# Optimization experiments

Hardware: AMD Instinct MI355X
Metric: run time of the kernel (lower is better)

Reference implementation:

```python
import jax, jax.numpy as jnp
import numpy as np

B, C, W, H, D = 4, 32, 64, 64, 64


def setup_inputs() -> dict:
    key = jax.random.key(0)
    ks = jax.random.split(key, 8)
    x = jax.random.normal(ks[0], (B, C, W, H, D), dtype=jnp.float32)
    # 1x1x1 Conv3d == per-voxel channel mixing: weight (C_out, C_in), bias (C_out,)
    Wq = jax.random.normal(ks[1], (C, C), dtype=jnp.float32) * 0.05
    bq = jax.random.normal(ks[2], (C,), dtype=jnp.float32) * 0.05
    Wk = jax.random.normal(ks[3], (C, C), dtype=jnp.float32) * 0.05
    bk = jax.random.normal(ks[4], (C,), dtype=jnp.float32) * 0.05
    Wv = jax.random.normal(ks[5], (C, C), dtype=jnp.float32) * 0.05
    bv = jax.random.normal(ks[6], (C,), dtype=jnp.float32) * 0.05
    gamma = jnp.float32(0.1)  # torch inits to 0; nonzero so output depends on attention
    return {"x": x, "Wq": Wq, "bq": bq, "Wk": Wk, "bk": bk, "Wv": Wv, "bv": bv, "gamma": gamma}


def reference(x, Wq, bq, Wk, bk, Wv, bv, gamma):
    b, c, w, h, d = x.shape
    N = w * h * d

    def proj(Wt, bt):
        # 1x1x1 conv then torch's .view(b, -1, c): a raw row-major reshape of
        # (b, c, w, h, d) -> (b, N, c) that interleaves channel/spatial (faithful).
        y = jnp.einsum('oc,bcwhd->bowhd', Wt, x) + bt[None, :, None, None, None]
        return y.reshape(b, N, c)

    q = proj(Wq, bq)  # (b, N, c)
    k = proj(Wk, bk)
    v = proj(Wv, bv)
    s = jnp.einsum('bnc,bnd->bcd', q, k)          # q^T k: tiny (b, c, c)
    a = jax.nn.softmax(s, axis=-1)
    scores = jnp.einsum('bnc,bcd->bnd', v, a)     # (b, N, c)
    return x + gamma * scores.reshape(b, c, w, h, d)
```

## Files before the change

kernel.cpp:

```cpp
#include <hip/hip_runtime.h>

typedef __attribute__((ext_vector_type(8))) short bf16x8;
typedef __attribute__((ext_vector_type(4))) float f32x4;

#define MSP   262144
#define BATCH 4
#define NT    8
#define NBLK  128

#define CSF   264
#define WTILE (8 * CSF)

#define OFF_P  0
#define OFF_CS 4096

#define GLDS16(gsrc, ldst)                                               \
  __builtin_amdgcn_global_load_lds(                                      \
      (const __attribute__((address_space(1))) unsigned int*)(gsrc),     \
      (__attribute__((address_space(3))) unsigned int*)(ldst), 16, 0, 0)

__device__ __forceinline__ unsigned short f2bf(float f) {
  unsigned int u = __float_as_uint(f);
  u += 0x7fffu + ((u >> 16) & 1u);
  return (unsigned short)(u >> 16);
}
__device__ __forceinline__ void split2(float f, short* hi, short* lo) {
  unsigned int u = __float_as_uint(f);
  unsigned int uh = u + (0x7fffu + ((u >> 16) & 1u));
  *hi = (short)(uh >> 16);
  const float r = f - __uint_as_float(uh & 0xffff0000u);
  *lo = (short)(__float_as_uint(r) >> 16);
}

#define MFMA(A, B, C) __builtin_amdgcn_mfma_f32_16x16x32_bf16(A, B, C, 0, 0, 0)


__global__ __launch_bounds__(256) void pass1_kernel(
    const float* __restrict__ x, const float* __restrict__ Wq,
    const float* __restrict__ Wk, float* __restrict__ ws) {
  __shared__ float XT[8 * WTILE];
  __shared__ float UW[3072];
  const int tid = threadIdx.x;
  const int w = tid >> 6, l = tid & 63, lm = tid & 15, lb = (tid >> 4) & 3;
  const int b = blockIdx.y;
  const size_t xbase = (size_t)b * 32 * MSP;
  const int wbase = (blockIdx.x * 4 + w) * (NT * 64);

  const int srow = l >> 4;
  const int scol = (l & 15) * 4;
  float* wbuf0 = XT + (w * 2 + 0) * WTILE;
  float* wbuf1 = XT + (w * 2 + 1) * WTILE;

#pragma unroll
  for (int c = 0; c < 8; ++c)
    GLDS16(x + xbase + (size_t)(c * 4 + srow) * MSP + wbase + scol,
           wbuf0 + c * CSF);

  {
    float* WqL = UW;
    float* WkL = UW + 1024;
    for (int k = tid; k < 1024; k += 256) { WqL[k] = Wq[k]; WkL[k] = Wk[k]; }
    __syncthreads();
    float* UL = UW + 2048;
    for (int k = tid; k < 1024; k += 256) {
      const int aa = k >> 5, bb = k & 31;
      float s = 0.f;
#pragma unroll
      for (int ch = 0; ch < 32; ++ch)
        s = fmaf(WqL[ch * 32 + aa], WkL[ch * 32 + bb], s);
      UL[k] = s;
    }
    __syncthreads();
  }
  bf16x8 uh0, ul0, uh1, ul1;
  {
    const float* UL = UW + 2048;
#pragma unroll
    for (int r = 0; r < 8; ++r) {
      const int kk = (r < 4) ? lb * 4 + r : 16 + lb * 4 + (r - 4);
      short h, lo;
      split2(UL[lm * 32 + kk], &h, &lo);        uh0[r] = h; ul0[r] = lo;
      split2(UL[(16 + lm) * 32 + kk], &h, &lo); uh1[r] = h; ul1[r] = lo;
    }
  }

  int ldsoff[8];
#pragma unroll
  for (int r = 0; r < 8; ++r) {
    const int ch = (r < 4) ? lb * 4 + r : 16 + lb * 4 + (r - 4);
    ldsoff[r] = (ch >> 2) * CSF + (ch & 3) * 64 + lm;
  }

  f32x4 p00 = {0, 0, 0, 0}, p01 = {0, 0, 0, 0}, p10 = {0, 0, 0, 0}, p11 = {0, 0, 0, 0};
  float cs0[8], cs1[8];
#pragma unroll
  for (int r = 0; r < 8; ++r) { cs0[r] = 0.f; cs1[r] = 0.f; }

#pragma unroll 1
  for (int t = 0; t < NT; ++t) {
    const float* XB = (t & 1) ? wbuf1 : wbuf0;
    float* XN = (t & 1) ? wbuf0 : wbuf1;
    if (t + 1 < NT) {
      const int posn = wbase + (t + 1) * 64;
#pragma unroll
      for (int c = 0; c < 8; ++c)
        GLDS16(x + xbase + (size_t)(c * 4 + srow) * MSP + posn + scol,
               XN + c * CSF);
      asm volatile("s_waitcnt vmcnt(8)" ::: "memory");
    } else {
      asm volatile("s_waitcnt vmcnt(0)" ::: "memory");
    }
    __builtin_amdgcn_sched_barrier(0);

#pragma unroll
    for (int g2 = 0; g2 < 2; ++g2) {
      const int pl = g2 * 32;
      float xf0[8], xf1[8];
#pragma unroll
      for (int r = 0; r < 8; ++r) {
        xf0[r] = XB[ldsoff[r] + pl];
        xf1[r] = XB[ldsoff[r] + pl + 16];
      }
      bf16x8 xh0, xl0, xh1, xl1;
#pragma unroll
      for (int r = 0; r < 8; ++r) {
        short h, lo;
        split2(xf0[r], &h, &lo); xh0[r] = h; xl0[r] = lo;
        split2(xf1[r], &h, &lo); xh1[r] = h; xl1[r] = lo;
        cs0[r] += xf0[r];  cs1[r] += xf1[r];
      }

      f32x4 y00 = {0,0,0,0}, y01 = {0,0,0,0}, y10 = {0,0,0,0}, y11 = {0,0,0,0};
      y00 = MFMA(uh0, xh0, y00); y00 = MFMA(uh0, xl0, y00); y00 = MFMA(ul0, xh0, y00);
      y01 = MFMA(uh1, xh0, y01); y01 = MFMA(uh1, xl0, y01); y01 = MFMA(ul1, xh0, y01);
      y10 = MFMA(uh0, xh1, y10); y10 = MFMA(uh0, xl1, y10); y10 = MFMA(ul0, xh1, y10);
      y11 = MFMA(uh1, xh1, y11); y11 = MFMA(uh1, xl1, y11); y11 = MFMA(ul1, xh1, y11);

      bf16x8 yh0, yl0, yh1, yl1;
#pragma unroll
      for (int r = 0; r < 4; ++r) {
        short h, lo;
        split2(y00[r], &h, &lo); yh0[r] = h; yl0[r] = lo;
        split2(y10[r], &h, &lo); yh1[r] = h; yl1[r] = lo;
      }
#pragma unroll
      for (int r = 4; r < 8; ++r) {
        short h, lo;
        split2(y01[r - 4], &h, &lo); yh0[r] = h; yl0[r] = lo;
        split2(y11[r - 4], &h, &lo); yh1[r] = h; yl1[r] = lo;
      }

      p00 = MFMA(xh0, yh0, p00); p00 = MFMA(xh0, yl0, p00); p00 = MFMA(xl0, yh0, p00);
      p01 = MFMA(xh0, yh1, p01); p01 = MFMA(xh0, yl1, p01); p01 = MFMA(xl0, yh1, p01);
      p10 = MFMA(xh1, yh0, p10); p10 = MFMA(xh1, yl0, p10); p10 = MFMA(xl1, yh0, p10);
      p11 = MFMA(xh1, yh1, p11); p11 = MFMA(xh1, yl1, p11); p11 = MFMA(xl1, yh1, p11);
    }
  }

  __syncthreads();
  float* red = XT;
#pragma unroll
  for (int r = 0; r < 4; ++r) {
    red[w * 1024 + (lb * 4 + r) * 32 + lm]           = p00[r];
    red[w * 1024 + (lb * 4 + r) * 32 + 16 + lm]      = p01[r];
    red[w * 1024 + (16 + lb * 4 + r) * 32 + lm]      = p10[r];
    red[w * 1024 + (16 + lb * 4 + r) * 32 + 16 + lm] = p11[r];
  }
  __syncthreads();
  for (int k = tid; k < 1024; k += 256) {
    const float s = red[k] + red[1024 + k] + red[2048 + k] + red[3072 + k];
    atomicAdd(&ws[OFF_P + b * 1024 + k], s);
  }
  __syncthreads();
#pragma unroll
  for (int r = 0; r < 8; ++r) {
    const int ch = (r < 4) ? lb * 4 + r : 16 + lb * 4 + (r - 4);
    red[w * 1024 + ch * 32 + lm]      = cs0[r];
    red[w * 1024 + ch * 32 + 16 + lm] = cs1[r];
  }
  __syncthreads();
  for (int k = tid; k < 1024; k += 256) {
    const float s = red[k] + red[1024 + k] + red[2048 + k] + red[3072 + k];
    atomicAdd(&ws[OFF_CS + b * 1024 + k], s);
  }
}

__global__ __launch_bounds__(256) void pass2_kernel(
    const float* __restrict__ x, const float* __restrict__ Wq,
    const float* __restrict__ bq, const float* __restrict__ Wk,
    const float* __restrict__ bk, const float* __restrict__ Wv,
    const float* __restrict__ bv, const float* __restrict__ gm,
    const float* __restrict__ ws, float* __restrict__ out) {
  __shared__ float XT[8 * WTILE];
  __shared__ float Sm[1024];
  __shared__ float u_l[32], v_l[32], su_l[32], sv_l[32], ca_l[32];
  __shared__ float beta_l;

  const int tid = threadIdx.x;
  const int w = tid >> 6, l = tid & 63, lm = tid & 15, lb = (tid >> 4) & 3;
  const int b = blockIdx.y;
  const size_t xbase = (size_t)b * 32 * MSP;
  const int wbase = ((NBLK - 1 - blockIdx.x) * 4 + w) * (NT * 64);

  const int srow = l >> 4;
  const int scol = (l & 15) * 4;
  float* wbuf0 = XT + (w * 2 + 0) * WTILE;
  float* wbuf1 = XT + (w * 2 + 1) * WTILE;

#pragma unroll
  for (int c = 0; c < 8; ++c)
    GLDS16(x + xbase + (size_t)(c * 4 + srow) * MSP + wbase + scol,
           wbuf0 + c * CSF);

  if (tid < 32) {
    float u = 0.f;
#pragma unroll
    for (int ch = 0; ch < 32; ++ch) u = fmaf(Wq[ch * 32 + tid], bk[ch], u);
    u_l[tid] = u;
  } else if (tid < 64) {
    const int j = tid - 32;
    float v = 0.f;
#pragma unroll
    for (int ch = 0; ch < 32; ++ch) v = fmaf(bq[ch], Wk[ch * 32 + j], v);
    v_l[j] = v;
  } else if (tid == 64) {
    float bt = 0.f;
#pragma unroll
    for (int ch = 0; ch < 32; ++ch) bt = fmaf(bq[ch], bk[ch], bt);
    beta_l = bt;
  }
  __syncthreads();
  if (tid < 32) {
    float s = 0.f;
#pragma unroll
    for (int a = 0; a < 32; ++a)
      s = fmaf(u_l[a], ws[OFF_CS + b * 1024 + a * 32 + tid], s);
    su_l[tid] = s;
  } else if (tid < 64) {
    const int j = tid - 32;
    float s = 0.f;
#pragma unroll
    for (int a = 0; a < 32; ++a)
      s = fmaf(v_l[a], ws[OFF_CS + b * 1024 + a * 32 + j], s);
    sv_l[j] = s;
  }
  __syncthreads();
  {
    const int si = tid >> 3, sj0 = (tid & 7) * 4;
    float s4[4];
#pragma unroll
    for (int c = 0; c < 4; ++c)
      s4[c] = ws[OFF_P + b * 1024 + si * 32 + sj0 + c] + su_l[si] +
              sv_l[sj0 + c] + 8192.0f * beta_l;
    float mx = fmaxf(fmaxf(s4[0], s4[1]), fmaxf(s4[2], s4[3]));
    mx = fmaxf(mx, __shfl_xor(mx, 1, 8));
    mx = fmaxf(mx, __shfl_xor(mx, 2, 8));
    mx = fmaxf(mx, __shfl_xor(mx, 4, 8));
    float e4[4], sum = 0.f;
#pragma unroll
    for (int c = 0; c < 4; ++c) { e4[c] = expf(s4[c] - mx); sum += e4[c]; }
    sum += __shfl_xor(sum, 1, 8);
    sum += __shfl_xor(sum, 2, 8);
    sum += __shfl_xor(sum, 4, 8);
    const float inv = 1.0f / sum;
#pragma unroll
    for (int c = 0; c < 4; ++c) Sm[si * 32 + sj0 + c] = e4[c] * inv;
  }
  __syncthreads();
  if (tid < 32) {
    float c = 0.f;
#pragma unroll
    for (int ii = 0; ii < 32; ++ii) c += Sm[ii * 32 + tid];
    ca_l[tid] = c;
  }
  bf16x8 a0, a1, wv0, wv1;
#pragma unroll
  for (int r = 0; r < 8; ++r) {
    const int kk = (r < 4) ? lb * 4 + r : 16 + lb * 4 + (r - 4);
    a0[r]  = (short)f2bf(Sm[kk * 32 + lm]);
    a1[r]  = (short)f2bf(Sm[kk * 32 + 16 + lm]);
    wv0[r] = (short)f2bf(Wv[lm * 32 + kk]);
    wv1[r] = (short)f2bf(Wv[(16 + lm) * 32 + kk]);
  }
  __syncthreads();

  const float gamma = gm[0];
  const float bv0 = bv[lm], bv1 = bv[16 + lm];
  float i00[4], i01[4], i10[4], i11[4];
#pragma unroll
  for (int r = 0; r < 4; ++r) {
    const float c0 = ca_l[lb * 4 + r];
    const float c1 = ca_l[16 + lb * 4 + r];
    i00[r] = bv0 * c0; i01[r] = bv1 * c0;
    i10[r] = bv0 * c1; i11[r] = bv1 * c1;
  }

  int ldsoff[8];
#pragma unroll
  for (int r = 0; r < 8; ++r) {
    const int ch = (r < 4) ? lb * 4 + r : 16 + lb * 4 + (r - 4);
    ldsoff[r] = (ch >> 2) * CSF + (ch & 3) * 64 + lm;
  }
  int resoff[2][2];
#pragma unroll
  for (int CT = 0; CT < 2; ++CT)
#pragma unroll
    for (int MT = 0; MT < 2; ++MT)
      resoff[CT][MT] = (CT * 4 + (lm >> 2)) * CSF + (lm & 3) * 64 +
                       MT * 16 + lb * 4;

#pragma unroll 1
  for (int t = 0; t < NT; ++t) {
    float* XB = (t & 1) ? wbuf1 : wbuf0;
    float* XN = (t & 1) ? wbuf0 : wbuf1;
    if (t + 1 < NT) {
      const int posn = wbase + (t + 1) * 64;
#pragma unroll
      for (int c = 0; c < 8; ++c)
        GLDS16(x + xbase + (size_t)(c * 4 + srow) * MSP + posn + scol,
               XN + c * CSF);
      if (t == 0)
        asm volatile("s_waitcnt vmcnt(8)" ::: "memory");
      else
        asm volatile("s_waitcnt vmcnt(16)" ::: "memory");
    } else {
      asm volatile("s_waitcnt vmcnt(8)" ::: "memory");
    }
    __builtin_amdgcn_sched_barrier(0);
    const int post = wbase + t * 64;

#pragma unroll
    for (int g2 = 0; g2 < 2; ++g2) {
      const int pl = g2 * 32;
      bf16x8 xh0, xh1;
#pragma unroll
      for (int r = 0; r < 8; ++r) {
        xh0[r] = (short)f2bf(XB[ldsoff[r] + pl]);
        xh1[r] = (short)f2bf(XB[ldsoff[r] + pl + 16]);
      }
      f32x4 v00 = {0,0,0,0}, v01 = {0,0,0,0}, v10 = {0,0,0,0}, v11 = {0,0,0,0};
      v00 = MFMA(xh0, wv0, v00); v01 = MFMA(xh0, wv1, v01);
      v10 = MFMA(xh1, wv0, v10); v11 = MFMA(xh1, wv1, v11);

      bf16x8 vb0, vb1;
#pragma unroll
      for (int r = 0; r < 4; ++r) { vb0[r] = (short)f2bf(v00[r]); vb1[r] = (short)f2bf(v01[r]); }
#pragma unroll
      for (int r = 4; r < 8; ++r) { vb0[r] = (short)f2bf(v10[r - 4]); vb1[r] = (short)f2bf(v11[r - 4]); }

      f32x4 t00 = {i00[0], i00[1], i00[2], i00[3]};
      f32x4 t01 = {i01[0], i01[1], i01[2], i01[3]};
      f32x4 t10 = {i10[0], i10[1], i10[2], i10[3]};
      f32x4 t11 = {i11[0], i11[1], i11[2], i11[3]};
      t00 = MFMA(a0, vb0, t00); t01 = MFMA(a0, vb1, t01);
      t10 = MFMA(a1, vb0, t10); t11 = MFMA(a1, vb1, t11);

#define EPI(TT, MT, CT)                                                           \
      {                                                                           \
        float* p = &XB[resoff[CT][MT] + pl];                                      \
        const f32x4 xr = *reinterpret_cast<const f32x4*>(p);                      \
        f32x4 o;                                                                  \
        o[0] = fmaf(gamma, TT[0], xr[0]); o[1] = fmaf(gamma, TT[1], xr[1]);       \
        o[2] = fmaf(gamma, TT[2], xr[2]); o[3] = fmaf(gamma, TT[3], xr[3]);       \
        *reinterpret_cast<f32x4*>(p) = o;                                         \
      }
      EPI(t00, 0, 0); EPI(t01, 0, 1); EPI(t10, 1, 0); EPI(t11, 1, 1);
#undef EPI
    }

#pragma unroll
    for (int c = 0; c < 8; ++c) {
      const f32x4 o4 =
          *reinterpret_cast<const f32x4*>(&XB[c * CSF + srow * 64 + scol]);
      *reinterpret_cast<f32x4*>(
          out + xbase + (size_t)(c * 4 + srow) * MSP + post + scol) = o4;
    }
  }
}

extern "C" void kernel_launch(void* const* d_in, const int* in_sizes, int n_in,
                              void* d_out, int out_size, void* d_ws, size_t ws_size,
                              hipStream_t stream) {
  const float* x  = (const float*)d_in[0];
  const float* Wq = (const float*)d_in[1];
  const float* bq = (const float*)d_in[2];
  const float* Wk = (const float*)d_in[3];
  const float* bk = (const float*)d_in[4];
  const float* Wv = (const float*)d_in[5];
  const float* bv = (const float*)d_in[6];
  const float* gm = (const float*)d_in[7];
  float* out = (float*)d_out;
  float* ws  = (float*)d_ws;

  hipMemsetAsync(ws, 0, 8192 * sizeof(float), stream);
  pass1_kernel<<<dim3(NBLK, BATCH), 256, 0, stream>>>(x, Wq, Wk, ws);
  pass2_kernel<<<dim3(NBLK, BATCH), 256, 0, stream>>>(x, Wq, bq, Wk, bk, Wv, bv,
                                                      gm, ws, out);
}
```

Before: 82.09 us.

## Launch pass1/pass2 per batch so each batch's input stays cache-resident

Replaces the two batched grid launches with a host loop that runs pass1 then pass2 once per batch. The batch index moves into pointer offsets on x, out and the workspace. The likely aim is for pass2 to reread a batch's 32 MB of x while it is still in the large last-level cache, rather than after all four batches have streamed through. NT is halved so each per-batch grid still has 256 blocks, and pass2 no longer walks blocks in reverse order. The cost is six extra kernel launches and the gaps between them.

```diff
diff --git a/kernel.cpp b/kernel.cpp
--- a/kernel.cpp
+++ b/kernel.cpp
@@ -5,8 +5,8 @@
 
 #define MSP   262144
 #define BATCH 4
-#define NT    8
-#define NBLK  128
+#define NT    4
+#define NBLK  (MSP / (4 * NT * 64))
 
 #define CSF   264
 #define WTILE (8 * CSF)
@@ -42,8 +42,6 @@
   __shared__ float UW[3072];
   const int tid = threadIdx.x;
   const int w = tid >> 6, l = tid & 63, lm = tid & 15, lb = (tid >> 4) & 3;
-  const int b = blockIdx.y;
-  const size_t xbase = (size_t)b * 32 * MSP;
   const int wbase = (blockIdx.x * 4 + w) * (NT * 64);
 
   const int srow = l >> 4;
@@ -53,8 +51,7 @@
 
 #pragma unroll
   for (int c = 0; c < 8; ++c)
-    GLDS16(x + xbase + (size_t)(c * 4 + srow) * MSP + wbase + scol,
-           wbuf0 + c * CSF);
+    GLDS16(x + (size_t)(c * 4 + srow) * MSP + wbase + scol, wbuf0 + c * CSF);
 
   {
     float* WqL = UW;
@@ -104,8 +101,7 @@
       const int posn = wbase + (t + 1) * 64;
 #pragma unroll
       for (int c = 0; c < 8; ++c)
-        GLDS16(x + xbase + (size_t)(c * 4 + srow) * MSP + posn + scol,
-               XN + c * CSF);
+        GLDS16(x + (size_t)(c * 4 + srow) * MSP + posn + scol, XN + c * CSF);
       asm volatile("s_waitcnt vmcnt(8)" ::: "memory");
     } else {
       asm volatile("s_waitcnt vmcnt(0)" ::: "memory");
@@ -169,7 +165,7 @@
   __syncthreads();
   for (int k = tid; k < 1024; k += 256) {
     const float s = red[k] + red[1024 + k] + red[2048 + k] + red[3072 + k];
-    atomicAdd(&ws[OFF_P + b * 1024 + k], s);
+    atomicAdd(&ws[OFF_P + k], s);
   }
   __syncthreads();
 #pragma unroll
@@ -181,7 +177,7 @@
   __syncthreads();
   for (int k = tid; k < 1024; k += 256) {
     const float s = red[k] + red[1024 + k] + red[2048 + k] + red[3072 + k];
-    atomicAdd(&ws[OFF_CS + b * 1024 + k], s);
+    atomicAdd(&ws[OFF_CS + k], s);
   }
 }
 
@@ -198,9 +194,7 @@
 
   const int tid = threadIdx.x;
   const int w = tid >> 6, l = tid & 63, lm = tid & 15, lb = (tid >> 4) & 3;
-  const int b = blockIdx.y;
-  const size_t xbase = (size_t)b * 32 * MSP;
-  const int wbase = ((NBLK - 1 - blockIdx.x) * 4 + w) * (NT * 64);
+  const int wbase = (blockIdx.x * 4 + w) * (NT * 64);
 
   const int srow = l >> 4;
   const int scol = (l & 15) * 4;
@@ -209,8 +203,7 @@
 
 #pragma unroll
   for (int c = 0; c < 8; ++c)
-    GLDS16(x + xbase + (size_t)(c * 4 + srow) * MSP + wbase + scol,
-           wbuf0 + c * CSF);
+    GLDS16(x + (size_t)(c * 4 + srow) * MSP + wbase + scol, wbuf0 + c * CSF);
 
   if (tid < 32) {
     float u = 0.f;
@@ -234,14 +227,14 @@
     float s = 0.f;
 #pragma unroll
     for (int a = 0; a < 32; ++a)
-      s = fmaf(u_l[a], ws[OFF_CS + b * 1024 + a * 32 + tid], s);
+      s = fmaf(u_l[a], ws[OFF_CS + a * 32 + tid], s);
     su_l[tid] = s;
   } else if (tid < 64) {
     const int j = tid - 32;
     float s = 0.f;
 #pragma unroll
     for (int a = 0; a < 32; ++a)
-      s = fmaf(v_l[a], ws[OFF_CS + b * 1024 + a * 32 + j], s);
+      s = fmaf(v_l[a], ws[OFF_CS + a * 32 + j], s);
     sv_l[j] = s;
   }
   __syncthreads();
@@ -250,7 +243,7 @@
     float s4[4];
 #pragma unroll
     for (int c = 0; c < 4; ++c)
-      s4[c] = ws[OFF_P + b * 1024 + si * 32 + sj0 + c] + su_l[si] +
+      s4[c] = ws[OFF_P + si * 32 + sj0 + c] + su_l[si] +
               sv_l[sj0 + c] + 8192.0f * beta_l;
     float mx = fmaxf(fmaxf(s4[0], s4[1]), fmaxf(s4[2], s4[3]));
     mx = fmaxf(mx, __shfl_xor(mx, 1, 8));
@@ -317,8 +310,7 @@
       const int posn = wbase + (t + 1) * 64;
 #pragma unroll
       for (int c = 0; c < 8; ++c)
-        GLDS16(x + xbase + (size_t)(c * 4 + srow) * MSP + posn + scol,
-               XN + c * CSF);
+        GLDS16(x + (size_t)(c * 4 + srow) * MSP + posn + scol, XN + c * CSF);
       if (t == 0)
         asm volatile("s_waitcnt vmcnt(8)" ::: "memory");
       else
@@ -371,9 +363,9 @@
 #pragma unroll
     for (int c = 0; c < 8; ++c) {
       const f32x4 o4 =
-          *reinterpret_cast<const f32x4*>(&XB[c * CSF + srow * 64 + scol]);
+          *reinterpret_cast<const f32x4*>(&XT[(size_t)(XB - XT) + c * CSF + srow * 64 + scol]);
       *reinterpret_cast<f32x4*>(
-          out + xbase + (size_t)(c * 4 + srow) * MSP + post + scol) = o4;
+          out + (size_t)(c * 4 + srow) * MSP + post + scol) = o4;
     }
   }
 }
@@ -393,7 +385,13 @@
   float* ws  = (float*)d_ws;
 
   hipMemsetAsync(ws, 0, 8192 * sizeof(float), stream);
-  pass1_kernel<<<dim3(NBLK, BATCH), 256, 0, stream>>>(x, Wq, Wk, ws);
-  pass2_kernel<<<dim3(NBLK, BATCH), 256, 0, stream>>>(x, Wq, bq, Wk, bk, Wv, bv,
-                                                      gm, ws, out);
-}
+
+  for (int b = 0; b < BATCH; ++b) {
+    const float* xb  = x   + (size_t)b * 32 * MSP;
+    float*       ob  = out + (size_t)b * 32 * MSP;
+    float*       wsb = ws  + b * 1024;
+    pass1_kernel<<<NBLK, 256, 0, stream>>>(xb, Wq, Wk, wsb);
+    pass2_kernel<<<NBLK, 256, 0, stream>>>(xb, Wq, bq, Wk, bk, Wv, bv, gm,
+                                           wsb, ob);
+  }
+}
```

Result: slower. 144.4 us (+75.9%).
